# Kernel optimization log

Measured on AMD Instinct MI355X. Metric: run time of the kernel, lower is better.

Reference implementation:

```python
import jax, jax.numpy as jnp
from jax import lax
import numpy as np

B, T, I, H, L, O = 256, 512, 1, 256, 4, 1


def setup_inputs() -> dict:
    key = jax.random.key(0)
    ks = jax.random.split(key, 4 * L + 3)
    s = 1.0 / np.sqrt(H)
    inp = {"x": jax.random.normal(ks[0], (B, T, I), dtype=jnp.float32)}
    for l in range(L):
        in_dim = I if l == 0 else H
        inp[f"W_ih{l}"] = jax.random.uniform(ks[1 + 4 * l], (4 * H, in_dim), minval=-s, maxval=s, dtype=jnp.float32)
        inp[f"W_hh{l}"] = jax.random.uniform(ks[2 + 4 * l], (4 * H, H), minval=-s, maxval=s, dtype=jnp.float32)
        inp[f"b_ih{l}"] = jax.random.uniform(ks[3 + 4 * l], (4 * H,), minval=-s, maxval=s, dtype=jnp.float32)
        inp[f"b_hh{l}"] = jax.random.uniform(ks[4 + 4 * l], (4 * H,), minval=-s, maxval=s, dtype=jnp.float32)
    inp["fc_W"] = jax.random.uniform(ks[-2], (O, H), minval=-s, maxval=s, dtype=jnp.float32)
    inp["fc_b"] = jax.random.uniform(ks[-1], (O,), minval=-s, maxval=s, dtype=jnp.float32)
    return inp


def _lstm_layer(x_seq, W_ih, W_hh, b_ih, b_hh):
    # x_seq: [B, T, in_dim] -> hidden sequence [B, T, H]
    b, t = x_seq.shape[0], x_seq.shape[1]
    h = W_hh.shape[1]
    # precompute input projections for all timesteps: [T, B, 4H]
    xg = jnp.einsum('bti,gi->tbg', x_seq, W_ih) + b_ih + b_hh

    def step(carry, xg_t):
        hp, cp = carry
        gates = xg_t + hp @ W_hh.T  # [B, 4H]
        i, f, g, o = jnp.split(gates, 4, axis=-1)  # PyTorch gate order: i,f,g,o
        i = jax.nn.sigmoid(i)
        f = jax.nn.sigmoid(f)
        g = jnp.tanh(g)
        o = jax.nn.sigmoid(o)
        c = f * cp + i * g
        hn = o * jnp.tanh(c)
        return (hn, c), hn

    h0 = jnp.zeros((b, h), x_seq.dtype)
    _, hs = lax.scan(step, (h0, h0), xg)
    return jnp.transpose(hs, (1, 0, 2))  # [B, T, H]


def reference(x, W_ih0, W_hh0, b_ih0, b_hh0, W_ih1, W_hh1, b_ih1, b_hh1,
              W_ih2, W_hh2, b_ih2, b_hh2, W_ih3, W_hh3, b_ih3, b_hh3, fc_W, fc_b):
    layers = [(W_ih0, W_hh0, b_ih0, b_hh0), (W_ih1, W_hh1, b_ih1, b_hh1),
              (W_ih2, W_hh2, b_ih2, b_hh2), (W_ih3, W_hh3, b_ih3, b_hh3)]
    out = x
    for Wi, Wh, bi, bh in layers:
        out = _lstm_layer(out, Wi, Wh, bi, bh)
    # final linear on last timestep hidden: [B, H] -> [B, O]
    return out[:, -1, :] @ fc_W.T + fc_b
```

## Files before the change

kernel.cpp:

```cpp
#include <hip/hip_runtime.h>
#include <stdint.h>

#define T_ 512
#define H_ 256
#define MB 32
#define NBUF 8
#define ISLOT 8192
#define NWG 256

typedef __attribute__((ext_vector_type(8))) short  short8;
typedef __attribute__((ext_vector_type(4))) float  floatx4;
typedef __attribute__((ext_vector_type(4))) unsigned int uint4v;
typedef unsigned long long ull;

struct Params {
  const float* x;
  const float* Wih[4]; const float* Whh[4]; const float* bih[4]; const float* bhh[4];
  const float* fcW; const float* fcb;
  int*   flags;
  int*   xcd;
  short* hring;
};

__device__ __forceinline__ short f2bf(float f){
  uint32_t u = __builtin_bit_cast(uint32_t, f);
  u += 0x7fffu + ((u >> 16) & 1u);
  return (short)(u >> 16);
}
__device__ __forceinline__ float bf2f(short s){
  uint32_t u = ((uint32_t)(uint16_t)s) << 16;
  return __builtin_bit_cast(float, u);
}
__device__ __forceinline__ float sigm(float v){ return 1.0f / (1.0f + __expf(-v)); }
__device__ __forceinline__ float tanh_(float v){
  float a = fabsf(v);
  float e = __expf(-2.0f * a);
  float r = (1.0f - e) / (1.0f + e);
  return v < 0.0f ? -r : r;
}

__device__ __forceinline__ void a_st32(unsigned* p, unsigned v){
  __hip_atomic_store(p, v, __ATOMIC_RELAXED, __HIP_MEMORY_SCOPE_AGENT);
}
__device__ __forceinline__ int a_ldi(const int* p){
  return __hip_atomic_load(p, __ATOMIC_RELAXED, __HIP_MEMORY_SCOPE_AGENT);
}
__device__ __forceinline__ void a_sti(int* p, int v){
  __hip_atomic_store(p, v, __ATOMIC_RELAXED, __HIP_MEMORY_SCOPE_AGENT);
}

__device__ __forceinline__ int ctr_poll(const int* p){
  int v; int z = 0;
  asm volatile("global_atomic_add %0, %1, %2, off sc0\n\t"
               "s_waitcnt vmcnt(0)"
               : "=v"(v) : "v"(p), "v"(z) : "memory");
  return v;
}
__device__ __forceinline__ void ctr_post(int* p){
  int one = 1;
  asm volatile("global_atomic_add %0, %1, off" :: "v"(p), "v"(one) : "memory");
}

template<bool SL> __device__ __forceinline__ void ld16t(uint4v& d, const void* p){
  if constexpr (SL) asm volatile("global_load_dwordx4 %0, %1, off sc0 sc1" : "=v"(d) : "v"(p));
  else              asm volatile("global_load_dwordx4 %0, %1, off sc0"     : "=v"(d) : "v"(p));
}
template<bool SL> __device__ __forceinline__ void st32t(unsigned* p, unsigned v){
  if constexpr (SL) a_st32(p, v);
  else asm volatile("global_store_dword %0, %1, off sc0" :: "v"(p), "v"(v) : "memory");
}
typedef __attribute__((address_space(1))) const void as1void;
typedef __attribute__((address_space(3))) void       as3void;
__device__ __forceinline__ void gld_lds16(const void* g, void* l){
  __builtin_amdgcn_global_load_lds((as1void*)g, (as3void*)l, 16, 0, 1);
}
__device__ __forceinline__ void inv_l1(){
  asm volatile("buffer_inv sc0" ::: "memory");
}

__device__ __forceinline__ void ldf32(float& d, const void* p){
  asm volatile("global_load_dword %0, %1, off" : "=v"(d) : "v"(p));
}
template<int N> __device__ __forceinline__ void waitvm(){
  if constexpr (N == 0) asm volatile("s_waitcnt vmcnt(0)" ::: "memory");
  else if constexpr (N == 1) asm volatile("s_waitcnt vmcnt(1)" ::: "memory");
  else                       asm volatile("s_waitcnt vmcnt(4)" ::: "memory");
}
__device__ __forceinline__ void bar_lds(){
  asm volatile("s_waitcnt lgkmcnt(0)" ::: "memory");
  __builtin_amdgcn_s_barrier();
}
__device__ __forceinline__ void bar_only(){
  __builtin_amdgcn_s_barrier();
}

#define MFMA(a,b,c) __builtin_amdgcn_mfma_f32_16x16x32_bf16((a),(b),(c),0,0,0)

__device__ __forceinline__ void wpoll(const int* p, int thr, bool& dead){
  if (dead) return;
  int guard = 0;
  for (;;){
    int v = a_ldi(p);
    if (__all((int)(v >= thr))) break;
    if (++guard > (1 << 16)) { dead = true; break; }
  }
}

__device__ __forceinline__ void cpoll(const int* self, const int* up, const int* down,
                                      int t, bool& dead){
  if (dead) return;
  const int lane = threadIdx.x & 63;
  const int* p = nullptr; int thr = 0;
  if (lane == 0)            { p = self; thr = t; }
  else if (lane == 1 && up) { p = up;   thr = t + 2; }
  else if (lane == 2 && down && ((t & 3) == 0)){ p = down; thr = t - 4; }
  if (thr > T_) thr = T_;
  thr <<= 3;
  int guard = 0;
  for (;;){
    int v = p ? ctr_poll(p) : 0x7fffffff;
    if (__all((int)(v >= thr))) break;
    __builtin_amdgcn_s_sleep(1);
    if (++guard > (1 << 14)) { dead = true; break; }
  }
}

template<bool L0, bool SL>
__device__ __forceinline__ void run_cell(const Params& p, int g, int l, int slice,
    short* a_frag, float (*g_lds)[MB][34], float (*bias_lds)[32],
    float (*wih0_lds)[32], float* x0_lds)
{
  constexpr int KBT = L0 ? 8 : 16;
  const int tid = threadIdx.x, lane = tid & 63, wave = tid >> 6;
  const int n15 = lane & 15, q4 = lane >> 4;

  int* fl_self = p.flags + (g * 4 + l) * 32;
  int* fl_up   = L0 ? fl_self : fl_self - 32;
  int* fl_down = (l < 3) ? fl_self + 32 : fl_self;
  short* hr_self = p.hring + (size_t)((g * 4 + l) * NBUF) * ISLOT;
  const short* hr_up = L0 ? (const short*)nullptr
                          : hr_self - (size_t)NBUF * ISLOT;

  int* ctr_self = fl_self;
  const int* ctr_up   = L0 ? (const int*)nullptr : fl_self - 32;
  const int* ctr_down = (l < 3) ? fl_self + 32 : (const int*)nullptr;

  if (tid < 128){
    int gt = tid >> 5, j = tid & 31;
    int gr = gt * 256 + slice * 32 + j;
    bias_lds[gt][j] = p.bih[l][gr] + p.bhh[l][gr];
    if (L0) wih0_lds[gt][j] = p.Wih[0][gr];
  }

  short8 wf0[KBT], wf1[KBT];
  const int g0 = wave * 256 + slice * 32 + n15;
  const int g1 = g0 + 16;
  #pragma unroll
  for (int kb = 0; kb < KBT; ++kb){
    const float* base; int kk;
    if (L0)          { base = p.Whh[0]; kk = kb * 32 + q4 * 8; }
    else if (kb < 8) { base = p.Wih[l]; kk = kb * 32 + q4 * 8; }
    else             { base = p.Whh[l]; kk = (kb - 8) * 32 + q4 * 8; }
    const float* p0 = base + (size_t)g0 * H_ + kk;
    const float* p1 = base + (size_t)g1 * H_ + kk;
    short8 a, b;
    #pragma unroll
    for (int i = 0; i < 8; ++i){ a[i] = f2bf(p0[i]); b[i] = f2bf(p1[i]); }
    wf0[kb] = a; wf1[kb] = b;
  }

  float c00 = 0.f, c01 = 0.f, c10 = 0.f, c11 = 0.f;
  const int r0 = (tid >> 4) * 2, r1 = r0 + 1;
  const int pc = (tid & 15) * 2;

  const int* pp; int dlt;
  if (lane < 8)      { pp = fl_self + lane; dlt = 0; }
  else if (lane < 16){ if (L0){ pp = fl_self; dlt = -1000000; }
                       else   { pp = fl_up + (lane - 8); dlt = 2; } }
  else if (lane < 24){ if (l < 3){ pp = fl_down + (lane - 16); dlt = -7; }
                       else      { pp = fl_self; dlt = -1000000; } }
  else               { pp = fl_self + (lane & 7); dlt = -1000000; }
  bool dead = false;

  uint4v* fragv = (uint4v*)a_frag;
  uint4v px[4];
  float xcur = 0.f;


  if (!L0){
    if constexpr (SL){
      wpoll(fl_up + (lane & 7), 1, dead);
    } else {
      if (wave == 0) cpoll(ctr_self, ctr_up, ctr_down, -1, dead);
      __syncthreads();
      inv_l1();
    }
    const char* s = (const char*)hr_up;
    #pragma unroll
    for (int k = 0; k < 4; ++k) ld16t<SL>(px[k], s + (size_t)(k * 256 + tid) * 16);
  } else if (wave == 0 && lane < MB){
    ldf32(xcur, &p.x[(size_t)(g * MB + lane) * T_]);
  }
  waitvm<0>();
  __syncthreads();

  for (int t = 0; t < T_; ++t){
    if constexpr (SL){
      int thr = t + dlt; if (thr > T_) thr = T_;
      wpoll(pp, thr, dead);
    } else {
      if (wave == 0) cpoll(ctr_self, ctr_up, ctr_down, t, dead);
    }

    if (!L0){
      #pragma unroll
      for (int k = 0; k < 4; ++k) fragv[k * 256 + tid] = px[k];
    } else if (wave == 0 && lane < MB){
      x0_lds[lane] = xcur;
    }

    const bool havh = (t > 0);
    const bool pf = (t + 1 < T_);
    const int hbase = L0 ? 0 : 1024;
    uint4v hv[4];

    if constexpr (SL){
      if (havh){
        const char* s = (const char*)(hr_self + (size_t)((t - 1) & 7) * ISLOT);
        #pragma unroll
        for (int k = 0; k < 4; ++k) ld16t<SL>(hv[k], s + (size_t)(k * 256 + tid) * 16);
      }
      if (!L0){
        if (pf){
          const char* s = (const char*)(hr_up + (size_t)((t + 1) & 7) * ISLOT);
          #pragma unroll
          for (int k = 0; k < 4; ++k) ld16t<SL>(px[k], s + (size_t)(k * 256 + tid) * 16);
        }
      } else if (wave == 0 && lane < MB && pf){
        ldf32(xcur, &p.x[(size_t)(g * MB + lane) * T_ + (t + 1)]);
      }
      bar_lds();
    } else {
      bar_lds();
      inv_l1();
      if (havh){
        const char* s = (const char*)(hr_self + (size_t)((t - 1) & 7) * ISLOT);
        #pragma unroll
        for (int k = 0; k < 4; ++k){
          const char* src = s + (size_t)(k * 256 + tid) * 16;
          gld_lds16(src, (void*)&fragv[hbase + k * 256 + (tid & ~63)]);
        }
      }
      if (!L0){
        if (pf){
          const char* s = (const char*)(hr_up + (size_t)((t + 1) & 7) * ISLOT);
          #pragma unroll
          for (int k = 0; k < 4; ++k) ld16t<SL>(px[k], s + (size_t)(k * 256 + tid) * 16);
        }
      } else if (wave == 0 && lane < MB && pf){
        ldf32(xcur, &p.x[(size_t)(g * MB + lane) * T_ + (t + 1)]);
      }
    }

    floatx4 acc[2][2][2] = {};
    if (!L0){
      #pragma unroll
      for (int kb = 0; kb < 8; ++kb){
        #pragma unroll
        for (int mt = 0; mt < 2; ++mt){
          short8 af = *(short8*)&a_frag[(kb * 2 + mt) * 512 + lane * 8];
          int pr = kb & 1;
          acc[mt][0][pr] = MFMA(af, wf0[kb], acc[mt][0][pr]);
          acc[mt][1][pr] = MFMA(af, wf1[kb], acc[mt][1][pr]);
        }
      }
    }

    if (!L0){ if (pf) waitvm<4>(); else waitvm<0>(); }
    else    { if (wave == 0 && pf) waitvm<1>(); else waitvm<0>(); }
    if constexpr (SL){
      if (havh){
        #pragma unroll
        for (int k = 0; k < 4; ++k) fragv[hbase + k * 256 + tid] = hv[k];
      } else {
        uint4v z = {0, 0, 0, 0};
        #pragma unroll
        for (int k = 0; k < 4; ++k) fragv[hbase + k * 256 + tid] = z;
      }
    } else {
      if (!havh){
        uint4v z = {0, 0, 0, 0};
        #pragma unroll
        for (int k = 0; k < 4; ++k) fragv[hbase + k * 256 + tid] = z;
      }
    }
    bar_lds();

    #pragma unroll
    for (int kb = (L0 ? 0 : 8); kb < KBT; ++kb){
      #pragma unroll
      for (int mt = 0; mt < 2; ++mt){
        short8 af = *(short8*)&a_frag[(kb * 2 + mt) * 512 + lane * 8];
        int pr = kb & 1;
        acc[mt][0][pr] = MFMA(af, wf0[kb], acc[mt][0][pr]);
        acc[mt][1][pr] = MFMA(af, wf1[kb], acc[mt][1][pr]);
      }
    }
    #pragma unroll
    for (int mt = 0; mt < 2; ++mt){
      floatx4 s0 = acc[mt][0][0] + acc[mt][0][1];
      floatx4 s1 = acc[mt][1][0] + acc[mt][1][1];
      int mrow = mt * 16 + q4 * 4;
      #pragma unroll
      for (int r = 0; r < 4; ++r){
        g_lds[wave][mrow + r][n15]      = s0[r];
        g_lds[wave][mrow + r][16 + n15] = s1[r];
      }
    }
    bar_lds();

    {
      float xs0 = 0.f, xs1 = 0.f;
      if (L0){ xs0 = x0_lds[r0]; xs1 = x0_lds[r1]; }
      float2 bi = *(const float2*)&bias_lds[0][pc];
      float2 bf = *(const float2*)&bias_lds[1][pc];
      float2 bg = *(const float2*)&bias_lds[2][pc];
      float2 bo = *(const float2*)&bias_lds[3][pc];
      float2 wi = {0.f,0.f}, wf = {0.f,0.f}, wg = {0.f,0.f}, wo = {0.f,0.f};
      if (L0){
        wi = *(const float2*)&wih0_lds[0][pc];
        wf = *(const float2*)&wih0_lds[1][pc];
        wg = *(const float2*)&wih0_lds[2][pc];
        wo = *(const float2*)&wih0_lds[3][pc];
      }
      short* slot = hr_self + (size_t)(t & 7) * ISLOT;
      #pragma unroll
      for (int rr = 0; rr < 2; ++rr){
        const int row = rr ? r1 : r0;
        const float xs = rr ? xs1 : xs0;
        float2 vi = *(const float2*)&g_lds[0][row][pc];
        float2 vf = *(const float2*)&g_lds[1][row][pc];
        float2 vg = *(const float2*)&g_lds[2][row][pc];
        float2 vo = *(const float2*)&g_lds[3][row][pc];
        float gi0 = vi.x + bi.x, gi1 = vi.y + bi.y;
        float gf0 = vf.x + bf.x, gf1 = vf.y + bf.y;
        float gg0 = vg.x + bg.x, gg1 = vg.y + bg.y;
        float go0 = vo.x + bo.x, go1 = vo.y + bo.y;
        if (L0){
          gi0 += xs * wi.x; gi1 += xs * wi.y;
          gf0 += xs * wf.x; gf1 += xs * wf.y;
          gg0 += xs * wg.x; gg1 += xs * wg.y;
          go0 += xs * wo.x; go1 += xs * wo.y;
        }
        float i0 = sigm(gi0), i1 = sigm(gi1);
        float f0 = sigm(gf0), f1 = sigm(gf1);
        float gv0 = tanh_(gg0), gv1 = tanh_(gg1);
        float o0 = sigm(go0), o1 = sigm(go1);
        float& ca = rr ? c10 : c00;
        float& cb = rr ? c11 : c01;
        ca = f0 * ca + i0 * gv0;
        cb = f1 * cb + i1 * gv1;
        float h0 = o0 * tanh_(ca);
        float h1 = o1 * tanh_(cb);
        unsigned pk = (unsigned)(uint16_t)f2bf(h0) | ((unsigned)(uint16_t)f2bf(h1) << 16);
        unsigned off = (unsigned)((slice * 2 + (row >> 4)) * 512
                     + ((pc >> 3) * 16 + (row & 15)) * 8 + (pc & 7));
        st32t<SL>((unsigned*)(slot + off), pk);
      }
    }

    waitvm<0>();
    bar_only();
    if (tid == 0){
      if constexpr (SL) a_sti(fl_self + slice, t + 1);
      else              ctr_post(ctr_self);
    }
  }
}

__global__ __launch_bounds__(256, 1) void lstm_kernel(Params p){
  __shared__ short a_frag[32 * 512];
  __shared__ float g_lds[4][MB][34];
  __shared__ float bias_lds[4][32];
  __shared__ float wih0_lds[4][32];
  __shared__ float x0_lds[MB];
  __shared__ int   fsh;

  const int bid   = blockIdx.x;
  const int g     = bid & 7;
  const int l     = (bid >> 3) & 3;
  const int slice = bid >> 5;

  int xcc;
  asm volatile("s_getreg_b32 %0, hwreg(HW_REG_XCC_ID)" : "=s"(xcc));
  const int me = xcc + 1;
  if (threadIdx.x == 0) a_sti(&p.xcd[bid], me);
  int fast;
  {
    const int lane = threadIdx.x & 63;
    const int idx = lane & 31;
    const int* xp = p.xcd + (idx >> 2) * 32 + (idx & 3) * 8 + g;
    int v = 0, guard = 0; bool giveup = false;
    for (;;){
      v = a_ldi(xp);
      if (__all((int)(v != 0))) break;
      if (++guard > (1 << 22)) { giveup = true; break; }
    }
    fast = (!giveup && __all((int)(v == me))) ? 1 : 0;
  }
  if (threadIdx.x == 0) fsh = 1;
  __syncthreads();
  if (!fast) fsh = 0;
  __syncthreads();
  fast = fsh;

  if (l == 0){
    if (fast) run_cell<true , false>(p, g, 0, slice, a_frag, g_lds, bias_lds, wih0_lds, x0_lds);
    else      run_cell<true , true >(p, g, 0, slice, a_frag, g_lds, bias_lds, wih0_lds, x0_lds);
  } else {
    if (fast) run_cell<false, false>(p, g, l, slice, a_frag, g_lds, bias_lds, wih0_lds, x0_lds);
    else      run_cell<false, true >(p, g, l, slice, a_frag, g_lds, bias_lds, wih0_lds, x0_lds);
  }
}

__global__ void fc_kernel(const short* __restrict__ hring, const float* __restrict__ fcW,
                          const float* __restrict__ fcb, float* __restrict__ out){
  int b = blockIdx.x, lane = threadIdx.x;
  int g = b >> 5, m = b & 31;
  int mt = m >> 4, mm = m & 15;
  const short* base = hring + (size_t)((g * 4 + 3) * NBUF + ((T_ - 1) & 7)) * ISLOT;
  float s = 0.f;
  #pragma unroll
  for (int k = 0; k < 4; ++k){
    int d = lane + 64 * k;
    int kb = d >> 5, koff = d & 31;
    short hv = base[(kb * 2 + mt) * 512 + ((koff >> 3) * 16 + mm) * 8 + (koff & 7)];
    s += bf2f(hv) * fcW[d];
  }
  #pragma unroll
  for (int off = 32; off; off >>= 1) s += __shfl_down(s, off);
  if (lane == 0) out[b] = s + fcb[0];
}

extern "C" void kernel_launch(void* const* d_in, const int* in_sizes, int n_in,
                              void* d_out, int out_size, void* d_ws, size_t ws_size,
                              hipStream_t stream) {
  Params P;
  P.x = (const float*)d_in[0];
  for (int l = 0; l < 4; ++l){
    P.Wih[l] = (const float*)d_in[1 + 4*l];
    P.Whh[l] = (const float*)d_in[2 + 4*l];
    P.bih[l] = (const float*)d_in[3 + 4*l];
    P.bhh[l] = (const float*)d_in[4 + 4*l];
  }
  P.fcW = (const float*)d_in[17];
  P.fcb = (const float*)d_in[18];

  char* ws = (char*)d_ws;
  P.flags = (int*)ws;
  P.xcd   = (int*)(ws + 4096);
  P.hring = (short*)(ws + 16384);

  hipMemsetAsync(ws, 0, 8192, stream);
  hipLaunchKernelGGL(lstm_kernel, dim3(NWG), dim3(256), 0, stream, P);
  hipLaunchKernelGGL(fc_kernel, dim3(256), dim3(64), 0, stream,
                     P.hring, P.fcW, P.fcb, (float*)d_out);
}
```

Measured before the change: 1.653 ms.

## Overlap input-projection MFMAs with counter polling in non-SL layer path

In the counter-polling (non-SL) path for layers above the first, the upper-layer input fragment is now written to LDS and half of the input-projection MFMAs run before waiting on the cross-workgroup counter. After the poll and the L1 invalidate, the own-hidden-state loads are issued and the other half of the input MFMAs runs while those loads are in flight. The aim is to hide poll and global-load latency on the serial recurrence critical path. The cost is an extra barrier per step and a more intricate ordering between the LDS fragment writes and the cross-workgroup synchronisation.

After: 1.536 ms (median of 2 runs). 1.08x faster.

```diff
diff --git a/kernel.cpp b/kernel.cpp
--- a/kernel.cpp
+++ b/kernel.cpp
@@ -186,7 +186,6 @@
   uint4v px[4];
   float xcur = 0.f;
 
-
   if (!L0){
     if constexpr (SL){
       wpoll(fl_up + (lane & 7), 1, dead);
@@ -205,26 +204,21 @@
   __syncthreads();
 
   for (int t = 0; t < T_; ++t){
-    if constexpr (SL){
-      int thr = t + dlt; if (thr > T_) thr = T_;
-      wpoll(pp, thr, dead);
-    } else {
-      if (wave == 0) cpoll(ctr_self, ctr_up, ctr_down, t, dead);
-    }
-
-    if (!L0){
-      #pragma unroll
-      for (int k = 0; k < 4; ++k) fragv[k * 256 + tid] = px[k];
-    } else if (wave == 0 && lane < MB){
-      x0_lds[lane] = xcur;
-    }
-
     const bool havh = (t > 0);
     const bool pf = (t + 1 < T_);
     const int hbase = L0 ? 0 : 1024;
     uint4v hv[4];
+    floatx4 acc[2][2][2] = {};
 
     if constexpr (SL){
+      { int thr = t + dlt; if (thr > T_) thr = T_;
+        wpoll(pp, thr, dead); }
+      if (!L0){
+        #pragma unroll
+        for (int k = 0; k < 4; ++k) fragv[k * 256 + tid] = px[k];
+      } else if (wave == 0 && lane < MB){
+        x0_lds[lane] = xcur;
+      }
       if (havh){
         const char* s = (const char*)(hr_self + (size_t)((t - 1) & 7) * ISLOT);
         #pragma unroll
@@ -240,32 +234,35 @@
         ldf32(xcur, &p.x[(size_t)(g * MB + lane) * T_ + (t + 1)]);
       }
       bar_lds();
-    } else {
+      if (!L0){
+        #pragma unroll
+        for (int kb = 0; kb < 8; ++kb){
+          #pragma unroll
+          for (int mt = 0; mt < 2; ++mt){
+            short8 af = *(short8*)&a_frag[(kb * 2 + mt) * 512 + lane * 8];
+            int pr = kb & 1;
+            acc[mt][0][pr] = MFMA(af, wf0[kb], acc[mt][0][pr]);
+            acc[mt][1][pr] = MFMA(af, wf1[kb], acc[mt][1][pr]);
+          }
+        }
+      }
+      if (!L0){ if (pf) waitvm<4>(); else waitvm<0>(); }
+      else    { if (wave == 0 && pf) waitvm<1>(); else waitvm<0>(); }
+      if (havh){
+        #pragma unroll
+        for (int k = 0; k < 4; ++k) fragv[hbase + k * 256 + tid] = hv[k];
+      } else {
+        uint4v z = {0, 0, 0, 0};
+        #pragma unroll
+        for (int k = 0; k < 4; ++k) fragv[hbase + k * 256 + tid] = z;
+      }
       bar_lds();
-      inv_l1();
-      if (havh){
-        const char* s = (const char*)(hr_self + (size_t)((t - 1) & 7) * ISLOT);
-        #pragma unroll
-        for (int k = 0; k < 4; ++k){
-          const char* src = s + (size_t)(k * 256 + tid) * 16;
-          gld_lds16(src, (void*)&fragv[hbase + k * 256 + (tid & ~63)]);
-        }
-      }
-      if (!L0){
-        if (pf){
-          const char* s = (const char*)(hr_up + (size_t)((t + 1) & 7) * ISLOT);
-          #pragma unroll
-          for (int k = 0; k < 4; ++k) ld16t<SL>(px[k], s + (size_t)(k * 256 + tid) * 16);
-        }
-      } else if (wave == 0 && lane < MB && pf){
-        ldf32(xcur, &p.x[(size_t)(g * MB + lane) * T_ + (t + 1)]);
-      }
-    }
-
-    floatx4 acc[2][2][2] = {};
-    if (!L0){
+    } else if constexpr (!L0){
       #pragma unroll
-      for (int kb = 0; kb < 8; ++kb){
+      for (int k = 0; k < 4; ++k) fragv[k * 256 + tid] = px[k];
+      bar_lds();
+      #pragma unroll
+      for (int kb = 0; kb < 4; ++kb){
         #pragma unroll
         for (int mt = 0; mt < 2; ++mt){
           short8 af = *(short8*)&a_frag[(kb * 2 + mt) * 512 + lane * 8];
@@ -274,27 +271,63 @@
           acc[mt][1][pr] = MFMA(af, wf1[kb], acc[mt][1][pr]);
         }
       }
-    }
-
-    if (!L0){ if (pf) waitvm<4>(); else waitvm<0>(); }
-    else    { if (wave == 0 && pf) waitvm<1>(); else waitvm<0>(); }
-    if constexpr (SL){
+      if (wave == 0) cpoll(ctr_self, ctr_up, ctr_down, t, dead);
+      bar_only();
+      inv_l1();
       if (havh){
-        #pragma unroll
-        for (int k = 0; k < 4; ++k) fragv[hbase + k * 256 + tid] = hv[k];
-      } else {
-        uint4v z = {0, 0, 0, 0};
-        #pragma unroll
-        for (int k = 0; k < 4; ++k) fragv[hbase + k * 256 + tid] = z;
-      }
-    } else {
+        const char* s = (const char*)(hr_self + (size_t)((t - 1) & 7) * ISLOT);
+        #pragma unroll
+        for (int k = 0; k < 4; ++k){
+          const char* src = s + (size_t)(k * 256 + tid) * 16;
+          gld_lds16(src, (void*)&fragv[hbase + k * 256 + (tid & ~63)]);
+        }
+      }
+      if (pf){
+        const char* s = (const char*)(hr_up + (size_t)((t + 1) & 7) * ISLOT);
+        #pragma unroll
+        for (int k = 0; k < 4; ++k) ld16t<SL>(px[k], s + (size_t)(k * 256 + tid) * 16);
+      }
+      #pragma unroll
+      for (int kb = 4; kb < 8; ++kb){
+        #pragma unroll
+        for (int mt = 0; mt < 2; ++mt){
+          short8 af = *(short8*)&a_frag[(kb * 2 + mt) * 512 + lane * 8];
+          int pr = kb & 1;
+          acc[mt][0][pr] = MFMA(af, wf0[kb], acc[mt][0][pr]);
+          acc[mt][1][pr] = MFMA(af, wf1[kb], acc[mt][1][pr]);
+        }
+      }
+      if (pf) waitvm<4>(); else waitvm<0>();
       if (!havh){
         uint4v z = {0, 0, 0, 0};
         #pragma unroll
         for (int k = 0; k < 4; ++k) fragv[hbase + k * 256 + tid] = z;
       }
-    }
-    bar_lds();
+      bar_lds();
+    } else {
+      if (wave == 0) cpoll(ctr_self, ctr_up, ctr_down, t, dead);
+      if (wave == 0 && lane < MB) x0_lds[lane] = xcur;
+      bar_lds();
+      inv_l1();
+      if (havh){
+        const char* s = (const char*)(hr_self + (size_t)((t - 1) & 7) * ISLOT);
+        #pragma unroll
+        for (int k = 0; k < 4; ++k){
+          const char* src = s + (size_t)(k * 256 + tid) * 16;
+          gld_lds16(src, (void*)&fragv[hbase + k * 256 + (tid & ~63)]);
+        }
+      }
+      if (wave == 0 && lane < MB && pf){
+        ldf32(xcur, &p.x[(size_t)(g * MB + lane) * T_ + (t + 1)]);
+      }
+      if (wave == 0 && pf) waitvm<1>(); else waitvm<0>();
+      if (!havh){
+        uint4v z = {0, 0, 0, 0};
+        #pragma unroll
+        for (int k = 0; k < 4; ++k) fragv[hbase + k * 256 + tid] = z;
+      }
+      bar_lds();
+    }
 
     #pragma unroll
     for (int kb = (L0 ? 0 : 8); kb < KBT; ++kb){
```
